# Kernel tuning notes

Measured on AMD Instinct MI355X. Metric: run time of the kernel, lower is better.

Reference implementation:

```python
import jax, jax.numpy as jnp
import numpy as np

MAX_DIST = 32  # unidirectional T5-style bucketing: num_buckets = 33
N_HEAD, D_K, D_V = 8, 64, 64


def setup_inputs() -> dict:
    key = jax.random.key(0)
    ks = jax.random.split(key, 9)
    B, S, D = 4, 2048, 512
    q = jax.random.normal(ks[0], (B, S, D), dtype=jnp.float32)
    k = jax.random.normal(ks[1], (B, S, D), dtype=jnp.float32)
    v = jax.random.normal(ks[2], (B, S, D), dtype=jnp.float32)
    mask = jax.random.randint(ks[3], (B, 1, 1, S), 0, 2, dtype=jnp.int32)
    sc = 1.0 / np.sqrt(D)
    Wq = jax.random.normal(ks[4], (D, D), dtype=jnp.float32) * sc
    Wk = jax.random.normal(ks[5], (D, D), dtype=jnp.float32) * sc
    Wv = jax.random.normal(ks[6], (D, D), dtype=jnp.float32) * sc
    Wfc = jax.random.normal(ks[7], (D, D), dtype=jnp.float32) * sc
    rel_bias = jax.random.normal(ks[8], (MAX_DIST + 1, N_HEAD), dtype=jnp.float32)
    return {"q": q, "k": k, "v": v, "mask": mask, "Wq": Wq, "Wk": Wk,
            "Wv": Wv, "Wfc": Wfc, "rel_bias": rel_bias}


def _rel_pos_bias(rel_bias, seq_len):
    # unidirectional: bucket = clamp(max(context - memory, 0), 0, MAX_DIST)
    pos = jnp.arange(seq_len)
    n = pos[:, None] - pos[None, :]              # context - memory = -relative_position
    bucket = jnp.clip(jnp.maximum(n, 0), 0, MAX_DIST)
    vals = rel_bias[bucket]                      # (S, S, H)
    return jnp.transpose(vals, (2, 0, 1))[None]  # (1, H, S, S)


def reference(q, k, v, mask, Wq, Wk, Wv, Wfc, rel_bias):
    B, Sq, _ = q.shape
    Sk = k.shape[1]
    scale = D_K ** (-0.5)
    qh = (q @ Wq).reshape(B, Sq, N_HEAD, D_K).transpose(0, 2, 1, 3)  # bhsd
    kh = (k @ Wk).reshape(B, Sk, N_HEAD, D_K).transpose(0, 2, 1, 3)
    vh = (v @ Wv).reshape(B, Sk, N_HEAD, D_V).transpose(0, 2, 1, 3)
    attn = jnp.einsum('bhqd,bhkd->bhqk', qh, kh) * scale
    attn = attn + _rel_pos_bias(rel_bias, Sq)
    attn = jnp.where(mask == 0, jnp.float32(-1e9), attn)
    attn = jax.nn.softmax(attn, axis=-1)          # dropout is identity at eval
    out = jnp.einsum('bhqk,bhkd->bhqd', attn, vh)
    out = out.transpose(0, 2, 1, 3).reshape(B, Sq, N_HEAD * D_V)
    out = out @ Wfc
    return out, attn
```

## Files before the change

### kernel.cpp

```cpp
#include <hip/hip_runtime.h>


typedef __attribute__((ext_vector_type(8))) short bfrag;
typedef __attribute__((ext_vector_type(4))) float f32x4;
typedef unsigned int u32;

#define MFMA16(a,b,c) __builtin_amdgcn_mfma_f32_16x16x32_bf16(a,b,c,0,0,0)

__device__ __forceinline__ void gl_lds16(const void* g, void* l){
  __builtin_amdgcn_global_load_lds((const __attribute__((address_space(1))) u32*)g,
                                   (__attribute__((address_space(3))) u32*)l, 16, 0, 0);
}
__device__ __forceinline__ short f2bs(float f){
  u32 u = __float_as_uint(f);
  u = (u + 0x7fffu + ((u>>16)&1u)) >> 16;
  return (short)u;
}
__device__ __forceinline__ float b2f(short s){
  return __uint_as_float(((u32)(unsigned short)s) << 16);
}

#define BB 4
#define HH 8
#define SS 2048
#define DD 512

#define WQT_OFF  0u
#define WKT_OFF  524288u
#define WVT_OFF  1048576u
#define WFCT_OFF 1572864u
#define QB_OFF   2097152u
#define KB_OFF   10485760u
#define VB_OFF   18874368u
#define QH_OFF   27262976u
#define KH_OFF   35651584u
#define VT_OFF   44040192u
#define OH_OFF   52428800u

__global__ __launch_bounds__(256) void conv_w_k(const float* w0,const float* w1,
                                                const float* w2,const float* w3, char* ws){
  const float* w; short* o;
  switch(blockIdx.z){
    case 0:  w=w0; o=(short*)(ws+WQT_OFF); break;
    case 1:  w=w1; o=(short*)(ws+WKT_OFF); break;
    case 2:  w=w2; o=(short*)(ws+WVT_OFF); break;
    default: w=w3; o=(short*)(ws+WFCT_OFF); break;
  }
  int t  = blockIdx.x*256 + threadIdx.x;
  int n  = t >> 6;
  int k0 = (t & 63) << 3;
  bfrag v;
  #pragma unroll
  for (int j=0;j<8;++j) v[j] = f2bs(w[(k0+j)*512 + n]);
  *(bfrag*)(o + n*512 + k0) = v;
}

__global__ __launch_bounds__(256) void conv_x_k(const float* x0,const float* x1,
                                                const float* x2, char* ws){
  const float* x; short* o;
  switch(blockIdx.z){
    case 0:  x=x0; o=(short*)(ws+QB_OFF); break;
    case 1:  x=x1; o=(short*)(ws+KB_OFF); break;
    default: x=x2; o=(short*)(ws+VB_OFF); break;
  }
  int i = (blockIdx.x*256 + threadIdx.x) << 3;
  float4 a = *(const float4*)(x+i);
  float4 b = *(const float4*)(x+i+4);
  bfrag v;
  v[0]=f2bs(a.x); v[1]=f2bs(a.y); v[2]=f2bs(a.z); v[3]=f2bs(a.w);
  v[4]=f2bs(b.x); v[5]=f2bs(b.y); v[6]=f2bs(b.z); v[7]=f2bs(b.w);
  *(bfrag*)(o+i) = v;
}

__device__ void gemm_core(const short* A, const short* Bt, char* Cout, int mode, int bid){
  __shared__ __align__(16) char lds[32768];
  int i0, j0;
  if (mode==1){ i0 = (bid&3)<<7; j0 = (bid>>2)<<7; }
  else        { i0 = (bid>>2)<<7; j0 = (bid&3)<<7; }
  int tid = threadIdx.x;
  int l = tid & 63, w = tid >> 6;
  int wr = (w>>1)<<6, wc = (w&1)<<6;
  int l15 = l & 15, l4 = l >> 4;
  f32x4 acc[4][4];
  #pragma unroll
  for(int a=0;a<4;++a)
    #pragma unroll
    for(int b=0;b<4;++b) acc[a][b] = (f32x4){0.f,0.f,0.f,0.f};
  const char* Ab = (const char*)A;
  const char* Bb = (const char*)Bt;
  for (int kk=0; kk<8; ++kk){
    #pragma unroll
    for (int it=0; it<4; ++it){
      int ci = it*256 + tid;
      int row = ci>>3, cc = ci&7;
      gl_lds16(Ab + (size_t)(i0+row)*1024 + kk*128 + ((cc^(row&7))<<4),
               lds + ((it*256 + w*64)<<4));
      gl_lds16(Bb + (size_t)(j0+row)*1024 + kk*128 + ((cc^(row&7))<<4),
               lds + 16384 + ((it*256 + w*64)<<4));
    }
    asm volatile("s_waitcnt vmcnt(0)" ::: "memory");
    __syncthreads();
    #pragma unroll
    for (int kb=0; kb<2; ++kb){
      bfrag af[4], bf[4];
      #pragma unroll
      for (int mi=0;mi<4;++mi){
        int row = wr + mi*16 + l15;
        af[mi] = *(const bfrag*)(lds + row*128 + (((kb*4 + l4) ^ (row&7))<<4));
      }
      #pragma unroll
      for (int ni=0;ni<4;++ni){
        int row = wc + ni*16 + l15;
        bf[ni] = *(const bfrag*)(lds + 16384 + row*128 + (((kb*4 + l4) ^ (row&7))<<4));
      }
      #pragma unroll
      for (int mi=0;mi<4;++mi)
        #pragma unroll
        for (int ni=0;ni<4;++ni)
          acc[mi][ni] = MFMA16(af[mi], bf[ni], acc[mi][ni]);
    }
    __syncthreads();
  }
  #pragma unroll
  for (int mi=0;mi<4;++mi){
    #pragma unroll
    for (int ni=0;ni<4;++ni){
      #pragma unroll
      for (int r=0;r<4;++r){
        int i = i0 + wr + mi*16 + (l4<<2) + r;
        int j = j0 + wc + ni*16 + l15;
        float v = acc[mi][ni][r];
        if (mode==2){
          ((float*)Cout)[(size_t)i*512 + j] = v;
        } else if (mode==0){
          size_t o = ((size_t)(((i>>11)<<3) + (j>>6))*2048 + (size_t)(i&2047))*64 + (j&63);
          ((short*)Cout)[o] = f2bs(v);
        } else {
          size_t o = ((size_t)(((j>>11)<<3) + (i>>6))*64 + (size_t)(i&63))*2048 + (j&2047);
          ((short*)Cout)[o] = f2bs(v);
        }
      }
    }
  }
}

__global__ __launch_bounds__(256,2) void gemm_proj_k(char* ws){
  switch(blockIdx.z){
    case 0:  gemm_core((const short*)(ws+QB_OFF),  (const short*)(ws+WQT_OFF), ws+QH_OFF, 0, blockIdx.x); break;
    case 1:  gemm_core((const short*)(ws+KB_OFF),  (const short*)(ws+WKT_OFF), ws+KH_OFF, 0, blockIdx.x); break;
    default: gemm_core((const short*)(ws+WVT_OFF), (const short*)(ws+VB_OFF),  ws+VT_OFF, 1, blockIdx.x); break;
  }
}
__global__ __launch_bounds__(256,2) void gemm_final_k(char* ws, float* out){
  gemm_core((const short*)(ws+OH_OFF), (const short*)(ws+WFCT_OFF), (char*)out, 2, blockIdx.x);
}

#define P_SZ      131072
#define KV_OFF_L  131072
#define MSK_OFF_L 147456
#define BIAS_OFF_L 155648
#define WSUM_OFF_L 155808
#define RECIP_OFF_L 156064
#define LDS_TOTAL  156192

__global__ __launch_bounds__(256,1) void attn_k(char* ws, const int* mask,
                                                const float* rel_bias, float* attn_out){
  extern __shared__ __align__(16) char sm[];
  int tid = threadIdx.x;
  int l = tid & 63, w = tid >> 6;
  int l15 = l & 15, l4 = l >> 4;
  int qblk = blockIdx.x, bh = blockIdx.y;
  int b = bh >> 3, h = bh & 7;
  const short* qhb = (const short*)(ws+QH_OFF) + (size_t)bh*SS*64;
  const char*  khb = ws + KH_OFF + (size_t)bh*SS*128;
  const char*  vtb = ws + VT_OFF + (size_t)bh*64*SS*2;

  {
    const int4* m4 = (const int4*)(mask + b*SS);
    int4 ma = m4[tid*2], mb = m4[tid*2+1];
    float4* mf = (float4*)(sm + MSK_OFF_L);
    mf[tid*2]   = make_float4(ma.x?1.f:0.f, ma.y?1.f:0.f, ma.z?1.f:0.f, ma.w?1.f:0.f);
    mf[tid*2+1] = make_float4(mb.x?1.f:0.f, mb.y?1.f:0.f, mb.z?1.f:0.f, mb.w?1.f:0.f);
  }
  if (tid < 33) ((float*)(sm+BIAS_OFF_L))[tid] = rel_bias[tid*HH + h];

  int wrow  = (w>>1)<<4;
  int qrow0 = (qblk<<5) + wrow;
  bfrag qf0 = *(const bfrag*)(qhb + (size_t)(qrow0 + l15)*64 + l4*8);
  bfrag qf1 = *(const bfrag*)(qhb + (size_t)(qrow0 + l15)*64 + 32 + l4*8);
  float rsum[4] = {0.f,0.f,0.f,0.f};
  char* kv0 = sm + KV_OFF_L;
  char* kv1 = sm + KV_OFF_L + 8192;
  const float* biasl = (const float*)(sm+BIAS_OFF_L);
  const float* maskl = (const float*)(sm+MSK_OFF_L);

  auto stageK = [&](int kc){
    const char* kt = khb + (size_t)kc*8192;
    char* dst = (kc&1)?kv1:kv0;
    #pragma unroll
    for (int it=0; it<2; ++it){
      int ci = it*256 + tid;
      int row = ci>>3, cc = ci&7;
      gl_lds16(kt + row*128 + ((cc^(row&7))<<4), dst + ((it*256 + w*64)<<4));
    }
  };
  auto stageV = [&](int vc){
    char* dst = (vc&1)?kv1:kv0;
    #pragma unroll
    for (int it=0; it<2; ++it){
      int ci = it*256 + tid;
      int row = ci>>3, cc = ci&7;
      gl_lds16(vtb + (size_t)row*4096 + (vc<<7) + ((cc^(row&7))<<4),
               dst + ((it*256 + w*64)<<4));
    }
  };

  stageK(0); stageK(1);
  __syncthreads();

  for (int kc=0; kc<32; ++kc){
    if (kc<31) { asm volatile("s_waitcnt vmcnt(2)" ::: "memory"); }
    else       { asm volatile("s_waitcnt vmcnt(0)" ::: "memory"); }
    __builtin_amdgcn_s_barrier();
    const char* kb = (kc&1)?kv1:kv0;
    int colb = (w&1)<<5;
    #pragma unroll
    for (int ct=0; ct<2; ++ct){
      int rowk = colb + (ct<<4) + l15;
      bfrag b0 = *(const bfrag*)(kb + rowk*128 + (((l4  )^(rowk&7))<<4));
      bfrag b1 = *(const bfrag*)(kb + rowk*128 + (((4+l4)^(rowk&7))<<4));
      f32x4 acc = (f32x4){0.f,0.f,0.f,0.f};
      acc = MFMA16(qf0, b0, acc);
      acc = MFMA16(qf1, b1, acc);
      int kpos = (kc<<6) + rowk;
      float mval = maskl[kpos];
      int rl0 = wrow + (l4<<2);
      int qg0 = (qblk<<5) + rl0;
      #pragma unroll
      for (int r=0;r<4;++r){
        int n = qg0 + r - kpos;
        n = n<0 ? 0 : (n>32 ? 32 : n);
        float s = acc[r]*0.125f + biasl[n];
        float p = mval * __expf(s);
        rsum[r] += p;
        int rowl = rl0 + r;
        int byte = kpos<<1;
        int ch = (byte>>4) ^ (rowl&15);
        *(short*)(sm + rowl*4096 + (ch<<4) + (byte&15)) = f2bs(p);
      }
    }
    __builtin_amdgcn_s_barrier();
    if (kc+2<32) stageK(kc+2);
  }

  stageV(0); stageV(1);

  {
    float* wsum = (float*)(sm+WSUM_OFF_L);
    #pragma unroll
    for (int r=0;r<4;++r){
      float s = rsum[r];
      s += __shfl_xor(s,1); s += __shfl_xor(s,2);
      s += __shfl_xor(s,4); s += __shfl_xor(s,8);
      if (l15==0) wsum[w*16 + (l4<<2) + r] = s;
    }
  }
  __syncthreads();
  if (tid < 32){
    float* wsum = (float*)(sm+WSUM_OFF_L);
    float t = (tid<16) ? (wsum[tid] + wsum[16+tid])
                       : (wsum[32+(tid&15)] + wsum[48+(tid&15)]);
    ((float*)(sm+RECIP_OFF_L))[tid] = 1.f/t;
  }
  __syncthreads();
  const float* recip = (const float*)(sm+RECIP_OFF_L);

  f32x4 acco0 = (f32x4){0.f,0.f,0.f,0.f}, acco1 = (f32x4){0.f,0.f,0.f,0.f};
  int dbase = (w&1)<<5;
  int prow = wrow + l15;
  for (int vc=0; vc<32; ++vc){
    if (vc<31) { asm volatile("s_waitcnt vmcnt(2)" ::: "memory"); }
    else       { asm volatile("s_waitcnt vmcnt(0)" ::: "memory"); }
    __builtin_amdgcn_s_barrier();
    const char* vb = (vc&1)?kv1:kv0;
    #pragma unroll
    for (int m=0;m<2;++m){
      int pcol = (vc<<6) + (m<<5) + (l4<<3);
      int pch = (pcol>>3) ^ (prow&15);
      bfrag af = *(const bfrag*)(sm + prow*4096 + (pch<<4));
      {
        int drow = dbase + l15;
        bfrag bv = *(const bfrag*)(vb + drow*128 + ((((m<<2)+l4)^(drow&7))<<4));
        acco0 = MFMA16(af, bv, acco0);
      }
      {
        int drow = dbase + 16 + l15;
        bfrag bv = *(const bfrag*)(vb + drow*128 + ((((m<<2)+l4)^(drow&7))<<4));
        acco1 = MFMA16(af, bv, acco1);
      }
    }
    __builtin_amdgcn_s_barrier();
    if (vc+2<32) stageV(vc+2);
  }

  {
    short* oh = (short*)(ws + OH_OFF);
    #pragma unroll
    for (int r=0;r<4;++r){
      int rowl = wrow + (l4<<2) + r;
      float rc = recip[rowl];
      size_t sg = (size_t)b*SS + (qblk<<5) + rowl;
      oh[sg*512 + h*64 + dbase + l15]      = f2bs(acco0[r]*rc);
      oh[sg*512 + h*64 + dbase + 16 + l15] = f2bs(acco1[r]*rc);
    }
  }

  {
    float* dst0 = attn_out + (size_t)bh*SS*SS + (size_t)(qblk<<5)*SS;
    #pragma unroll
    for (int rr=0; rr<8; ++rr){
      int rowl = (w<<3) + rr;
      float rc = recip[rowl];
      float* dst = dst0 + (size_t)rowl*SS;
      #pragma unroll
      for (int it=0; it<4; ++it){
        int col = it*512 + (l<<3);
        int ch = (col>>3) ^ (rowl&15);
        bfrag pv = *(const bfrag*)(sm + rowl*4096 + (ch<<4));
        f32x4 o0 = (f32x4){b2f(pv[0])*rc, b2f(pv[1])*rc, b2f(pv[2])*rc, b2f(pv[3])*rc};
        f32x4 o1 = (f32x4){b2f(pv[4])*rc, b2f(pv[5])*rc, b2f(pv[6])*rc, b2f(pv[7])*rc};
        __builtin_nontemporal_store(o0, (f32x4*)(dst+col));
        __builtin_nontemporal_store(o1, (f32x4*)(dst+col+4));
      }
    }
  }
}

extern "C" void kernel_launch(void* const* d_in, const int* in_sizes, int n_in,
                              void* d_out, int out_size, void* d_ws, size_t ws_size,
                              hipStream_t stream){
  const float* q   = (const float*)d_in[0];
  const float* k   = (const float*)d_in[1];
  const float* v   = (const float*)d_in[2];
  const int*  mask = (const int*)  d_in[3];
  const float* Wq  = (const float*)d_in[4];
  const float* Wk  = (const float*)d_in[5];
  const float* Wv  = (const float*)d_in[6];
  const float* Wfc = (const float*)d_in[7];
  const float* rb  = (const float*)d_in[8];
  char* ws = (char*)d_ws;
  float* out  = (float*)d_out;
  float* attn = out + (size_t)BB*SS*512;

  (void)hipFuncSetAttribute((const void*)attn_k,
        hipFuncAttributeMaxDynamicSharedMemorySize, LDS_TOTAL);

  conv_w_k<<<dim3(128,1,4), 256, 0, stream>>>(Wq, Wk, Wv, Wfc, ws);
  conv_x_k<<<dim3(2048,1,3), 256, 0, stream>>>(q, k, v, ws);
  gemm_proj_k<<<dim3(256,1,3), 256, 0, stream>>>(ws);
  attn_k<<<dim3(64,32), 256, LDS_TOTAL, stream>>>(ws, mask, rb, attn);
  gemm_final_k<<<dim3(256,1,1), 256, 0, stream>>>(ws, out);
}
```

Before: 398.2 us.

## Double attention block to 512 threads, splitting key/value columns across eight waves

The attention kernel now runs 8 waves per block instead of 4. Each wave handles one 16-column key slice in QK^T and one 16-wide head-dim slice in PV, so the per-thread loops shrink and each thread stages one K/V chunk instead of two. The row-sum reduction now combines four partial sums per row, and the attention-matrix write is spread over 8 waves. The intent is more latency hiding and more memory-level parallelism for the dominant attention output store, since LDS use limits occupancy to one block per CU. The cost is more barrier participants and more threads per barrier.

```diff
diff --git a/kernel.cpp b/kernel.cpp
--- a/kernel.cpp
+++ b/kernel.cpp
@@ -155,20 +155,20 @@
   gemm_core((const short*)(ws+OH_OFF), (const short*)(ws+WFCT_OFF), (char*)out, 2, blockIdx.x);
 }
 
-#define P_SZ      131072
-#define KV_OFF_L  131072
-#define MSK_OFF_L 147456
-#define BIAS_OFF_L 155648
-#define WSUM_OFF_L 155808
-#define RECIP_OFF_L 156064
-#define LDS_TOTAL  156192
-
-__global__ __launch_bounds__(256,1) void attn_k(char* ws, const int* mask,
+#define KV_OFF_L    131072
+#define MSK_OFF_L   147456
+#define BIAS_OFF_L  155648
+#define WSUM_OFF_L  155808
+#define RECIP_OFF_L 156320
+#define LDS_TOTAL   156448
+
+__global__ __launch_bounds__(512,1) void attn_k(char* ws, const int* mask,
                                                 const float* rel_bias, float* attn_out){
   extern __shared__ __align__(16) char sm[];
   int tid = threadIdx.x;
   int l = tid & 63, w = tid >> 6;
   int l15 = l & 15, l4 = l >> 4;
+  int wq = w >> 2, wk = w & 3;
   int qblk = blockIdx.x, bh = blockIdx.y;
   int b = bh >> 3, h = bh & 7;
   const short* qhb = (const short*)(ws+QH_OFF) + (size_t)bh*SS*64;
@@ -177,14 +177,13 @@
 
   {
     const int4* m4 = (const int4*)(mask + b*SS);
-    int4 ma = m4[tid*2], mb = m4[tid*2+1];
+    int4 ma = m4[tid];
     float4* mf = (float4*)(sm + MSK_OFF_L);
-    mf[tid*2]   = make_float4(ma.x?1.f:0.f, ma.y?1.f:0.f, ma.z?1.f:0.f, ma.w?1.f:0.f);
-    mf[tid*2+1] = make_float4(mb.x?1.f:0.f, mb.y?1.f:0.f, mb.z?1.f:0.f, mb.w?1.f:0.f);
+    mf[tid] = make_float4(ma.x?1.f:0.f, ma.y?1.f:0.f, ma.z?1.f:0.f, ma.w?1.f:0.f);
   }
   if (tid < 33) ((float*)(sm+BIAS_OFF_L))[tid] = rel_bias[tid*HH + h];
 
-  int wrow  = (w>>1)<<4;
+  int wrow  = wq << 4;
   int qrow0 = (qblk<<5) + wrow;
   bfrag qf0 = *(const bfrag*)(qhb + (size_t)(qrow0 + l15)*64 + l4*8);
   bfrag qf1 = *(const bfrag*)(qhb + (size_t)(qrow0 + l15)*64 + 32 + l4*8);
@@ -197,57 +196,45 @@
   auto stageK = [&](int kc){
     const char* kt = khb + (size_t)kc*8192;
     char* dst = (kc&1)?kv1:kv0;
-    #pragma unroll
-    for (int it=0; it<2; ++it){
-      int ci = it*256 + tid;
-      int row = ci>>3, cc = ci&7;
-      gl_lds16(kt + row*128 + ((cc^(row&7))<<4), dst + ((it*256 + w*64)<<4));
-    }
+    int row = tid>>3, cc = tid&7;
+    gl_lds16(kt + row*128 + ((cc^(row&7))<<4), dst + (tid<<4));
   };
   auto stageV = [&](int vc){
     char* dst = (vc&1)?kv1:kv0;
-    #pragma unroll
-    for (int it=0; it<2; ++it){
-      int ci = it*256 + tid;
-      int row = ci>>3, cc = ci&7;
-      gl_lds16(vtb + (size_t)row*4096 + (vc<<7) + ((cc^(row&7))<<4),
-               dst + ((it*256 + w*64)<<4));
-    }
+    int row = tid>>3, cc = tid&7;
+    gl_lds16(vtb + (size_t)row*4096 + (vc<<7) + ((cc^(row&7))<<4),
+             dst + (tid<<4));
   };
 
   stageK(0); stageK(1);
   __syncthreads();
 
   for (int kc=0; kc<32; ++kc){
-    if (kc<31) { asm volatile("s_waitcnt vmcnt(2)" ::: "memory"); }
+    if (kc<31) { asm volatile("s_waitcnt vmcnt(1)" ::: "memory"); }
     else       { asm volatile("s_waitcnt vmcnt(0)" ::: "memory"); }
     __builtin_amdgcn_s_barrier();
     const char* kb = (kc&1)?kv1:kv0;
-    int colb = (w&1)<<5;
-    #pragma unroll
-    for (int ct=0; ct<2; ++ct){
-      int rowk = colb + (ct<<4) + l15;
-      bfrag b0 = *(const bfrag*)(kb + rowk*128 + (((l4  )^(rowk&7))<<4));
-      bfrag b1 = *(const bfrag*)(kb + rowk*128 + (((4+l4)^(rowk&7))<<4));
-      f32x4 acc = (f32x4){0.f,0.f,0.f,0.f};
-      acc = MFMA16(qf0, b0, acc);
-      acc = MFMA16(qf1, b1, acc);
-      int kpos = (kc<<6) + rowk;
-      float mval = maskl[kpos];
-      int rl0 = wrow + (l4<<2);
-      int qg0 = (qblk<<5) + rl0;
-      #pragma unroll
-      for (int r=0;r<4;++r){
-        int n = qg0 + r - kpos;
-        n = n<0 ? 0 : (n>32 ? 32 : n);
-        float s = acc[r]*0.125f + biasl[n];
-        float p = mval * __expf(s);
-        rsum[r] += p;
-        int rowl = rl0 + r;
-        int byte = kpos<<1;
-        int ch = (byte>>4) ^ (rowl&15);
-        *(short*)(sm + rowl*4096 + (ch<<4) + (byte&15)) = f2bs(p);
-      }
+    int rowk = (wk<<4) + l15;
+    bfrag b0 = *(const bfrag*)(kb + rowk*128 + (((l4  )^(rowk&7))<<4));
+    bfrag b1 = *(const bfrag*)(kb + rowk*128 + (((4+l4)^(rowk&7))<<4));
+    f32x4 acc = (f32x4){0.f,0.f,0.f,0.f};
+    acc = MFMA16(qf0, b0, acc);
+    acc = MFMA16(qf1, b1, acc);
+    int kpos = (kc<<6) + rowk;
+    float mval = maskl[kpos];
+    int rl0 = wrow + (l4<<2);
+    int qg0 = (qblk<<5) + rl0;
+    #pragma unroll
+    for (int r=0;r<4;++r){
+      int n = qg0 + r - kpos;
+      n = n<0 ? 0 : (n>32 ? 32 : n);
+      float s = acc[r]*0.125f + biasl[n];
+      float p = mval * __expf(s);
+      rsum[r] += p;
+      int rowl = rl0 + r;
+      int byte = kpos<<1;
+      int ch = (byte>>4) ^ (rowl&15);
+      *(short*)(sm + rowl*4096 + (ch<<4) + (byte&15)) = f2bs(p);
     }
     __builtin_amdgcn_s_barrier();
     if (kc+2<32) stageK(kc+2);
@@ -268,18 +255,19 @@
   __syncthreads();
   if (tid < 32){
     float* wsum = (float*)(sm+WSUM_OFF_L);
-    float t = (tid<16) ? (wsum[tid] + wsum[16+tid])
-                       : (wsum[32+(tid&15)] + wsum[48+(tid&15)]);
+    int iq = tid >> 4, i = tid & 15;
+    float t = wsum[(iq*4+0)*16 + i] + wsum[(iq*4+1)*16 + i]
+            + wsum[(iq*4+2)*16 + i] + wsum[(iq*4+3)*16 + i];
     ((float*)(sm+RECIP_OFF_L))[tid] = 1.f/t;
   }
   __syncthreads();
   const float* recip = (const float*)(sm+RECIP_OFF_L);
 
-  f32x4 acco0 = (f32x4){0.f,0.f,0.f,0.f}, acco1 = (f32x4){0.f,0.f,0.f,0.f};
-  int dbase = (w&1)<<5;
+  f32x4 acco = (f32x4){0.f,0.f,0.f,0.f};
+  int dbase = wk << 4;
   int prow = wrow + l15;
   for (int vc=0; vc<32; ++vc){
-    if (vc<31) { asm volatile("s_waitcnt vmcnt(2)" ::: "memory"); }
+    if (vc<31) { asm volatile("s_waitcnt vmcnt(1)" ::: "memory"); }
     else       { asm volatile("s_waitcnt vmcnt(0)" ::: "memory"); }
     __builtin_amdgcn_s_barrier();
     const char* vb = (vc&1)?kv1:kv0;
@@ -288,16 +276,9 @@
       int pcol = (vc<<6) + (m<<5) + (l4<<3);
       int pch = (pcol>>3) ^ (prow&15);
       bfrag af = *(const bfrag*)(sm + prow*4096 + (pch<<4));
-      {
-        int drow = dbase + l15;
-        bfrag bv = *(const bfrag*)(vb + drow*128 + ((((m<<2)+l4)^(drow&7))<<4));
-        acco0 = MFMA16(af, bv, acco0);
-      }
-      {
-        int drow = dbase + 16 + l15;
-        bfrag bv = *(const bfrag*)(vb + drow*128 + ((((m<<2)+l4)^(drow&7))<<4));
-        acco1 = MFMA16(af, bv, acco1);
-      }
+      int drow = dbase + l15;
+      bfrag bv = *(const bfrag*)(vb + drow*128 + ((((m<<2)+l4)^(drow&7))<<4));
+      acco = MFMA16(af, bv, acco);
     }
     __builtin_amdgcn_s_barrier();
     if (vc+2<32) stageV(vc+2);
@@ -310,16 +291,15 @@
       int rowl = wrow + (l4<<2) + r;
       float rc = recip[rowl];
       size_t sg = (size_t)b*SS + (qblk<<5) + rowl;
-      oh[sg*512 + h*64 + dbase + l15]      = f2bs(acco0[r]*rc);
-      oh[sg*512 + h*64 + dbase + 16 + l15] = f2bs(acco1[r]*rc);
+      oh[sg*512 + h*64 + dbase + l15] = f2bs(acco[r]*rc);
     }
   }
 
   {
     float* dst0 = attn_out + (size_t)bh*SS*SS + (size_t)(qblk<<5)*SS;
     #pragma unroll
-    for (int rr=0; rr<8; ++rr){
-      int rowl = (w<<3) + rr;
+    for (int rr=0; rr<4; ++rr){
+      int rowl = (w<<2) + rr;
       float rc = recip[rowl];
       float* dst = dst0 + (size_t)rowl*SS;
       #pragma unroll
@@ -358,6 +338,6 @@
   conv_w_k<<<dim3(128,1,4), 256, 0, stream>>>(Wq, Wk, Wv, Wfc, ws);
   conv_x_k<<<dim3(2048,1,3), 256, 0, stream>>>(q, k, v, ws);
   gemm_proj_k<<<dim3(256,1,3), 256, 0, stream>>>(ws);
-  attn_k<<<dim3(64,32), 256, LDS_TOTAL, stream>>>(ws, mask, rb, attn);
+  attn_k<<<dim3(64,32), 512, LDS_TOTAL, stream>>>(ws, mask, rb, attn);
   gemm_final_k<<<dim3(256,1,1), 256, 0, stream>>>(ws, out);
 }
```

New measurement: 366.3 us. 8.0% less time.
